# Optimization experiments

Measured on AMD Instinct MI355X. Metric: run time of the kernel, lower is better.

Reference implementation:

```python
import jax, jax.numpy as jnp
import numpy as np


def _prelu(x, a):
    # nn.PReLU() with a single learnable parameter a
    return jnp.where(x >= 0, x, a * x)


def _conv1x1(x, w, b):
    # x: [n, cin, h, w], w: [cout, cin], b: [cout]
    return jnp.einsum('nchw,oc->nohw', x, w) + b[None, :, None, None]


def setup_inputs() -> dict:
    key = jax.random.key(0)
    ks = jax.random.split(key, 7)
    N, C, H, W = 8, 64, 64, 64
    red = 2
    c = C // red
    s = 1.0 / np.sqrt(C).astype(np.float32)
    x = jax.random.normal(ks[0], (N, C, H, W), dtype=jnp.float32)
    w1 = jax.random.normal(ks[1], (c, C), dtype=jnp.float32) * s
    b1 = jnp.zeros((c,), dtype=jnp.float32)
    w2 = jax.random.normal(ks[2], (c, C), dtype=jnp.float32) * s
    b2 = jnp.zeros((c,), dtype=jnp.float32)
    w3 = jax.random.normal(ks[3], (C, C), dtype=jnp.float32) * s
    b3 = jnp.zeros((C,), dtype=jnp.float32)
    a1 = jnp.full((1,), 0.25, dtype=jnp.float32)
    a2 = jnp.full((1,), 0.25, dtype=jnp.float32)
    a3 = jnp.full((1,), 0.25, dtype=jnp.float32)
    return {"x": x, "w1": w1, "b1": b1, "a1": a1, "w2": w2, "b2": b2,
            "a2": a2, "w3": w3, "b3": b3, "a3": a3}


def reference(x, w1, b1, a1, w2, b2, a2, w3, b3, a3):
    res_scale = 1.0
    n, C, h, w = x.shape
    e1 = _prelu(_conv1x1(x, w1, b1), a1[0])  # [n, c, h, w]
    e2 = _prelu(_conv1x1(x, w2, b2), a2[0])  # [n, c, h, w]
    e3 = _prelu(_conv1x1(x, w3, b3), a3[0])  # [n, C, h, w]
    c = e1.shape[1]
    hw = h * w
    q = e1.transpose(0, 2, 3, 1).reshape(n, hw, c)   # [n, hw, c]
    k = e2.reshape(n, c, hw)                         # [n, c, hw]
    score = jax.nn.softmax(jnp.matmul(q, k), axis=-1)  # [n, hw, hw]
    v = e3.reshape(n, C, hw).transpose(0, 2, 1)      # [n, hw, C]
    out = jnp.matmul(score, v)                       # [n, hw, C]
    out = out.transpose(0, 2, 1).reshape(n, C, h, w)
    return out + res_scale * x
```

## Files before the change

### kernel.cpp

```cpp
#include <hip/hip_runtime.h>
#include <hip/hip_bf16.h>

typedef __bf16 bf16x8 __attribute__((ext_vector_type(8)));
typedef float  f32x4  __attribute__((ext_vector_type(4)));
typedef float  f32x16 __attribute__((ext_vector_type(16)));
typedef int    i32x4  __attribute__((ext_vector_type(4)));

#define SEQ 4096
#define CIN 64
#define KSPLIT 8
#define KCHUNK (SEQ / KSPLIT)
#define NT32 (KCHUNK / 32)
#define LOG2E 1.44269504088896340736f

__device__ __forceinline__ unsigned cvtpk(float lo, float hi) {
    unsigned r;
    asm("v_cvt_pk_bf16_f32 %0, %1, %2" : "=v"(r) : "v"(lo), "v"(hi));
    return r;
}

__global__ __launch_bounds__(256, 2) void qkv_gen(
    const float* __restrict__ x,
    const float* __restrict__ w1, const float* __restrict__ b1, const float* __restrict__ a1,
    const float* __restrict__ w2, const float* __restrict__ b2, const float* __restrict__ a2,
    const float* __restrict__ w3, const float* __restrict__ b3, const float* __restrict__ a3,
    __bf16* __restrict__ qws, __bf16* __restrict__ kws, __bf16* __restrict__ vtws)
{
    __shared__ float xs[CIN][64];
    __shared__ float wl[CIN][128];
    __shared__ float bl[128];
    __shared__ float al[4];

    const int t  = threadIdx.x;
    const int n  = blockIdx.x >> 6;
    const int p0 = (blockIdx.x & 63) << 6;

    for (int idx = t; idx < 2048; idx += 256) {
        int j = idx >> 6, c = idx & 63;
        wl[c][j]      = w1[idx];
        wl[c][32 + j] = w2[idx];
    }
    for (int idx = t; idx < 4096; idx += 256) {
        int j = idx >> 6, c = idx & 63;
        wl[c][64 + j] = w3[idx];
    }
    if (t < 32) { bl[t] = b1[t]; bl[32 + t] = b2[t]; }
    if (t >= 128 && t < 192) bl[64 + (t - 128)] = b3[t - 128];
    if (t == 0) { al[0] = a1[0]; al[1] = a2[0]; al[2] = a3[0]; }

    const float* xb = x + ((size_t)n * CIN) * SEQ + p0;
    for (int r = 0; r < 16; ++r) {
        int e = r * 256 + t;
        xs[e >> 6][e & 63] = xb[(size_t)(e >> 6) * SEQ + (e & 63)];
    }
    __syncthreads();

    const int p  = t & 63;
    const int g  = t >> 6;
    const int jb = g << 5;
    const float a = (g == 0) ? al[0] : ((g == 1) ? al[1] : al[2]);

    float acc[32];
    #pragma unroll
    for (int j = 0; j < 32; ++j) acc[j] = bl[jb + j];

    for (int c = 0; c < CIN; ++c) {
        float xv = xs[c][p];
        const f32x4* wr = (const f32x4*)&wl[c][jb];
        #pragma unroll
        for (int j4 = 0; j4 < 8; ++j4) {
            f32x4 wv = wr[j4];
            acc[j4*4+0] = fmaf(wv[0], xv, acc[j4*4+0]);
            acc[j4*4+1] = fmaf(wv[1], xv, acc[j4*4+1]);
            acc[j4*4+2] = fmaf(wv[2], xv, acc[j4*4+2]);
            acc[j4*4+3] = fmaf(wv[3], xv, acc[j4*4+3]);
        }
    }
    #pragma unroll
    for (int j = 0; j < 32; ++j) acc[j] = acc[j] >= 0.f ? acc[j] : a * acc[j];

    const int pg = p0 + p;
    if (g <= 1) {
        const float sc = (g == 0) ? LOG2E : 1.0f;
        __bf16* dst = (g == 0 ? qws : kws) + ((size_t)n * SEQ + pg) * 32;
        #pragma unroll
        for (int v8 = 0; v8 < 4; ++v8) {
            bf16x8 o;
            #pragma unroll
            for (int i = 0; i < 8; ++i) o[i] = (__bf16)(acc[v8*8+i] * sc);
            *(bf16x8*)(dst + v8*8) = o;
        }
    } else {
        __bf16* dst = vtws + (size_t)n * (256 * 1024)
                      + (size_t)(pg >> 4) * 1024 + (jb - 64) * 16 + (pg & 15);
        #pragma unroll
        for (int j = 0; j < 32; ++j) dst[j * 16] = (__bf16)acc[j];
    }
}

template<int ATOMIC>
__global__ __launch_bounds__(256, 4) void attn(
    const __bf16* __restrict__ qws, const __bf16* __restrict__ kws,
    const __bf16* __restrict__ vtws,
    void* __restrict__ Ows, float* __restrict__ lws)
{
    const int t    = threadIdx.x;
    const int lane = t & 63;
    const int n    = blockIdx.x & 7;
    const int qblk = (blockIdx.x >> 3) & 31;
    const int ks   = blockIdx.x >> 8;
    const int wid  = t >> 6;
    const int l31  = lane & 31;
    const int h    = lane >> 5;
    const int qbase = qblk * 128 + wid * 32;
    const int kbase = ks * KCHUNK;
    const int koff = l31 * 64 + h * 16;
    const int voff = l31 * 32 + h * 16;

    const char* kb = (const char*)(kws + (size_t)n * SEQ * 32) + (size_t)kbase * 64;
    const char* vb = (const char*)(vtws + (size_t)n * (256 * 1024))
                     + (size_t)(kbase >> 4) * 2048;

    const char* qp = (const char*)(qws + (size_t)n * SEQ * 32)
                     + (size_t)(qbase + l31) * 64 + h * 16;
    const bf16x8 qf0 = *(const bf16x8*)(qp);
    const bf16x8 qf1 = *(const bf16x8*)(qp + 32);

    f32x16 of0 = {}, of1 = {};
    f32x4 ls4 = {0.f, 0.f, 0.f, 0.f};

    #pragma unroll 2
    for (int tile = 0; tile < NT32; ++tile) {
        const char* kp = kb + (size_t)tile * 2048;
        const char* vp = vb + (size_t)tile * 4096;

        bf16x8 kfa  = *(const bf16x8*)(kp + koff);
        bf16x8 kfb  = *(const bf16x8*)(kp + koff + 32);
        bf16x8 vf00 = *(const bf16x8*)(vp + voff);
        bf16x8 vf01 = *(const bf16x8*)(vp + voff + 1024);
        bf16x8 vf10 = *(const bf16x8*)(vp + voff + 2048);
        bf16x8 vf11 = *(const bf16x8*)(vp + voff + 3072);

        f32x16 s = {};
        s = __builtin_amdgcn_mfma_f32_32x32x16_bf16(kfa, qf0, s, 0, 0, 0);
        s = __builtin_amdgcn_mfma_f32_32x32x16_bf16(kfb, qf1, s, 0, 0, 0);

        float p[16];
        #pragma unroll
        for (int r = 0; r < 16; ++r) p[r] = __builtin_exp2f(s[r]);
        f32x4 e0 = { p[0], p[1], p[2],  p[3]  };
        f32x4 e1 = { p[4], p[5], p[6],  p[7]  };
        f32x4 e2 = { p[8], p[9], p[10], p[11] };
        f32x4 e3 = { p[12], p[13], p[14], p[15] };
        ls4 += e0 + e1 + e2 + e3;

        unsigned c[8];
        #pragma unroll
        for (int j = 0; j < 4; ++j) {
            c[j]     = cvtpk(p[2*j],     p[2*j + 1]);
            c[4 + j] = cvtpk(p[8 + 2*j], p[9 + 2*j]);
        }
        asm("v_permlane32_swap_b32 %0, %1" : "+v"(c[0]), "+v"(c[2]));
        asm("v_permlane32_swap_b32 %0, %1" : "+v"(c[1]), "+v"(c[3]));
        asm("v_permlane32_swap_b32 %0, %1" : "+v"(c[4]), "+v"(c[6]));
        asm("v_permlane32_swap_b32 %0, %1" : "+v"(c[5]), "+v"(c[7]));

        i32x4 b0 = { (int)c[0], (int)c[1], (int)c[2], (int)c[3] };
        i32x4 b1 = { (int)c[4], (int)c[5], (int)c[6], (int)c[7] };
        bf16x8 pf0 = __builtin_bit_cast(bf16x8, b0);
        bf16x8 pf1 = __builtin_bit_cast(bf16x8, b1);
        of0 = __builtin_amdgcn_mfma_f32_32x32x16_bf16(vf00, pf0, of0, 0, 0, 0);
        of1 = __builtin_amdgcn_mfma_f32_32x32x16_bf16(vf01, pf0, of1, 0, 0, 0);
        of0 = __builtin_amdgcn_mfma_f32_32x32x16_bf16(vf10, pf1, of0, 0, 0, 0);
        of1 = __builtin_amdgcn_mfma_f32_32x32x16_bf16(vf11, pf1, of1, 0, 0, 0);
    }

    const float ls = ls4[0] + ls4[1] + ls4[2] + ls4[3];
    const int qg = qbase + l31;
    if (ATOMIC) {
        float* Ob = (float*)Ows + (size_t)n * CIN * SEQ;
        #pragma unroll
        for (int r = 0; r < 16; ++r) {
            int dv = (r & 3) + 8 * (r >> 2) + 4 * h;
            unsafeAtomicAdd(Ob + (size_t)dv * SEQ + qg,        of0[r]);
            unsafeAtomicAdd(Ob + (size_t)(dv + 32) * SEQ + qg, of1[r]);
        }
        unsafeAtomicAdd(lws + n * SEQ + qg, ls);
    } else {
        __bf16* Ob = (__bf16*)Ows + (size_t)ks * (8 * CIN * SEQ) + (size_t)n * CIN * SEQ;
        #pragma unroll
        for (int r = 0; r < 16; ++r) {
            int dv = (r & 3) + 8 * (r >> 2) + 4 * h;
            Ob[(size_t)dv * SEQ + qg]        = (__bf16)of0[r];
            Ob[(size_t)(dv + 32) * SEQ + qg] = (__bf16)of1[r];
        }
        float lt = ls + __shfl_xor(ls, 32);
        if (h == 0) lws[(size_t)ks * (8 * SEQ) + n * SEQ + qg] = lt;
    }
}

__global__ __launch_bounds__(256) void lred(float* __restrict__ lws)
{
    int i = blockIdx.x * 256 + threadIdx.x;
    float s = 0.f;
    #pragma unroll
    for (int ks = 0; ks < KSPLIT; ++ks) s += lws[ks * 32768 + i];
    lws[i] = 1.f / s;
}

__global__ __launch_bounds__(256) void combine8(
    const __bf16* __restrict__ O8, const float* __restrict__ linv,
    const float* __restrict__ x, float* __restrict__ out)
{
    const int i = blockIdx.x * 256 + threadIdx.x;
    const int q8 = i & 511;
    const int nd = i >> 9;
    const int n  = nd >> 6;

    float o[8] = {};
    const __bf16* base = O8 + (size_t)nd * SEQ + q8 * 8;
    #pragma unroll
    for (int ks = 0; ks < KSPLIT; ++ks) {
        bf16x8 v = *(const bf16x8*)(base + (size_t)ks * (8 * CIN * SEQ));
        #pragma unroll
        for (int j = 0; j < 8; ++j) o[j] += (float)v[j];
    }
    const float* ivp = linv + n * SEQ + q8 * 8;
    f32x4 iv0 = *(const f32x4*)(ivp);
    f32x4 iv1 = *(const f32x4*)(ivp + 4);
    const float* xp = x + (size_t)nd * SEQ + q8 * 8;
    f32x4 x0 = *(const f32x4*)(xp);
    f32x4 x1 = *(const f32x4*)(xp + 4);
    f32x4 r0, r1;
    r0[0] = o[0]*iv0[0] + x0[0]; r0[1] = o[1]*iv0[1] + x0[1];
    r0[2] = o[2]*iv0[2] + x0[2]; r0[3] = o[3]*iv0[3] + x0[3];
    r1[0] = o[4]*iv1[0] + x1[0]; r1[1] = o[5]*iv1[1] + x1[1];
    r1[2] = o[6]*iv1[2] + x1[2]; r1[3] = o[7]*iv1[3] + x1[3];
    float* op = out + (size_t)nd * SEQ + q8 * 8;
    *(f32x4*)(op)     = r0;
    *(f32x4*)(op + 4) = r1;
}

__global__ __launch_bounds__(256) void combine1(
    const float* __restrict__ Ows, const float* __restrict__ lws,
    const float* __restrict__ x, float* __restrict__ out)
{
    const int total = 8 * CIN * SEQ / 4;
    for (int i = blockIdx.x * 256 + threadIdx.x; i < total; i += gridDim.x * 256) {
        int q4 = i & 1023;
        int n  = i >> 16;
        f32x4 o4 = *(const f32x4*)(Ows + (size_t)i * 4);
        f32x4 l4 = *(const f32x4*)(lws + (size_t)n * SEQ + q4 * 4);
        f32x4 x4 = *(const f32x4*)(x + (size_t)i * 4);
        f32x4 r;
        r[0] = o4[0] / l4[0] + x4[0];
        r[1] = o4[1] / l4[1] + x4[1];
        r[2] = o4[2] / l4[2] + x4[2];
        r[3] = o4[3] / l4[3] + x4[3];
        *(f32x4*)(out + (size_t)i * 4) = r;
    }
}

extern "C" void kernel_launch(void* const* d_in, const int* in_sizes, int n_in,
                              void* d_out, int out_size, void* d_ws, size_t ws_size,
                              hipStream_t stream)
{
    (void)in_sizes; (void)n_in; (void)out_size;
    const float* x  = (const float*)d_in[0];
    const float* w1 = (const float*)d_in[1];
    const float* b1 = (const float*)d_in[2];
    const float* a1 = (const float*)d_in[3];
    const float* w2 = (const float*)d_in[4];
    const float* b2 = (const float*)d_in[5];
    const float* a2 = (const float*)d_in[6];
    const float* w3 = (const float*)d_in[7];
    const float* b3 = (const float*)d_in[8];
    const float* a3 = (const float*)d_in[9];
    float* out = (float*)d_out;

    char* ws = (char*)d_ws;
    __bf16* qws  = (__bf16*)(ws);
    __bf16* kws  = (__bf16*)(ws + (2u << 20));
    __bf16* vtws = (__bf16*)(ws + (4u << 20));

    hipLaunchKernelGGL(qkv_gen, dim3(512), dim3(256), 0, stream,
                       x, w1, b1, a1, w2, b2, a2, w3, b3, a3, qws, kws, vtws);

    const size_t need_split = (8u << 20) + (32u << 20) + (1u << 20);
    if (ws_size >= need_split) {
        __bf16* O8   = (__bf16*)(ws + (8u << 20));
        float*  lws8 = (float*)(ws + (40u << 20));
        hipLaunchKernelGGL(attn<0>, dim3(8 * 32 * KSPLIT), dim3(256), 0, stream,
                           qws, kws, vtws, (void*)O8, lws8);
        hipLaunchKernelGGL(lred, dim3(128), dim3(256), 0, stream, lws8);
        hipLaunchKernelGGL(combine8, dim3(1024), dim3(256), 0, stream,
                           O8, lws8, x, out);
    } else {
        float* Ows = (float*)(ws + (8u << 20));
        float* lws = (float*)(ws + (16u << 20));
        hipMemsetAsync(Ows, 0, (8u << 20) + (128u << 10), stream);
        hipLaunchKernelGGL(attn<1>, dim3(8 * 32 * KSPLIT), dim3(256), 0, stream,
                           qws, kws, vtws, (void*)Ows, lws);
        hipLaunchKernelGGL(combine1, dim3(1024), dim3(256), 0, stream,
                           Ows, lws, x, out);
    }
}
```

Before: 83.51 us.

## Software-pipeline attention K/V loads, raise MFMA priority, fold lred into combine

The attention inner loop now double-buffers its K/V fragment loads, issuing the next tile's global loads before computing the current tile, in place of a plain unroll-by-2. The MFMA sections are wrapped in s_setprio so matrix work gets scheduling priority over other waves. The separate row-sum reduction kernel is removed, and combine8 now sums the eight partial softmax denominators itself and divides directly. This saves one launch and one pass over lws, at the cost of more loads and divides per combine thread and higher register pressure from holding two fragment sets.

```diff
diff --git a/kernel.cpp b/kernel.cpp
--- a/kernel.cpp
+++ b/kernel.cpp
@@ -96,6 +96,25 @@
         #pragma unroll
         for (int j = 0; j < 32; ++j) dst[j * 16] = (__bf16)acc[j];
     }
+}
+
+struct Frags {
+    bf16x8 ka, kb, v00, v01, v10, v11;
+};
+
+__device__ __forceinline__ Frags ldf(const char* kb_, const char* vb_,
+                                     int tile, int koff, int voff)
+{
+    Frags f;
+    const char* kp = kb_ + (size_t)tile * 2048;
+    const char* vp = vb_ + (size_t)tile * 4096;
+    f.ka  = *(const bf16x8*)(kp + koff);
+    f.kb  = *(const bf16x8*)(kp + koff + 32);
+    f.v00 = *(const bf16x8*)(vp + voff);
+    f.v01 = *(const bf16x8*)(vp + voff + 1024);
+    f.v10 = *(const bf16x8*)(vp + voff + 2048);
+    f.v11 = *(const bf16x8*)(vp + voff + 3072);
+    return f;
 }
 
 template<int ATOMIC>
@@ -129,21 +148,12 @@
     f32x16 of0 = {}, of1 = {};
     f32x4 ls4 = {0.f, 0.f, 0.f, 0.f};
 
-    #pragma unroll 2
-    for (int tile = 0; tile < NT32; ++tile) {
-        const char* kp = kb + (size_t)tile * 2048;
-        const char* vp = vb + (size_t)tile * 4096;
-
-        bf16x8 kfa  = *(const bf16x8*)(kp + koff);
-        bf16x8 kfb  = *(const bf16x8*)(kp + koff + 32);
-        bf16x8 vf00 = *(const bf16x8*)(vp + voff);
-        bf16x8 vf01 = *(const bf16x8*)(vp + voff + 1024);
-        bf16x8 vf10 = *(const bf16x8*)(vp + voff + 2048);
-        bf16x8 vf11 = *(const bf16x8*)(vp + voff + 3072);
-
+    auto body = [&](const Frags& F) {
         f32x16 s = {};
-        s = __builtin_amdgcn_mfma_f32_32x32x16_bf16(kfa, qf0, s, 0, 0, 0);
-        s = __builtin_amdgcn_mfma_f32_32x32x16_bf16(kfb, qf1, s, 0, 0, 0);
+        __builtin_amdgcn_s_setprio(1);
+        s = __builtin_amdgcn_mfma_f32_32x32x16_bf16(F.ka, qf0, s, 0, 0, 0);
+        s = __builtin_amdgcn_mfma_f32_32x32x16_bf16(F.kb, qf1, s, 0, 0, 0);
+        __builtin_amdgcn_s_setprio(0);
 
         float p[16];
         #pragma unroll
@@ -169,10 +179,22 @@
         i32x4 b1 = { (int)c[4], (int)c[5], (int)c[6], (int)c[7] };
         bf16x8 pf0 = __builtin_bit_cast(bf16x8, b0);
         bf16x8 pf1 = __builtin_bit_cast(bf16x8, b1);
-        of0 = __builtin_amdgcn_mfma_f32_32x32x16_bf16(vf00, pf0, of0, 0, 0, 0);
-        of1 = __builtin_amdgcn_mfma_f32_32x32x16_bf16(vf01, pf0, of1, 0, 0, 0);
-        of0 = __builtin_amdgcn_mfma_f32_32x32x16_bf16(vf10, pf1, of0, 0, 0, 0);
-        of1 = __builtin_amdgcn_mfma_f32_32x32x16_bf16(vf11, pf1, of1, 0, 0, 0);
+        __builtin_amdgcn_s_setprio(1);
+        of0 = __builtin_amdgcn_mfma_f32_32x32x16_bf16(F.v00, pf0, of0, 0, 0, 0);
+        of1 = __builtin_amdgcn_mfma_f32_32x32x16_bf16(F.v01, pf0, of1, 0, 0, 0);
+        of0 = __builtin_amdgcn_mfma_f32_32x32x16_bf16(F.v10, pf1, of0, 0, 0, 0);
+        of1 = __builtin_amdgcn_mfma_f32_32x32x16_bf16(F.v11, pf1, of1, 0, 0, 0);
+        __builtin_amdgcn_s_setprio(0);
+    };
+
+    Frags A = ldf(kb, vb, 0, koff, voff);
+    #pragma unroll 1
+    for (int tile = 0; tile < NT32; tile += 2) {
+        Frags B = ldf(kb, vb, tile + 1, koff, voff);
+        body(A);
+        if (tile + 2 < NT32)
+            A = ldf(kb, vb, tile + 2, koff, voff);
+        body(B);
     }
 
     const float ls = ls4[0] + ls4[1] + ls4[2] + ls4[3];
@@ -199,17 +221,8 @@
     }
 }
 
-__global__ __launch_bounds__(256) void lred(float* __restrict__ lws)
-{
-    int i = blockIdx.x * 256 + threadIdx.x;
-    float s = 0.f;
-    #pragma unroll
-    for (int ks = 0; ks < KSPLIT; ++ks) s += lws[ks * 32768 + i];
-    lws[i] = 1.f / s;
-}
-
 __global__ __launch_bounds__(256) void combine8(
-    const __bf16* __restrict__ O8, const float* __restrict__ linv,
+    const __bf16* __restrict__ O8, const float* __restrict__ lws,
     const float* __restrict__ x, float* __restrict__ out)
 {
     const int i = blockIdx.x * 256 + threadIdx.x;
@@ -225,17 +238,25 @@
         #pragma unroll
         for (int j = 0; j < 8; ++j) o[j] += (float)v[j];
     }
-    const float* ivp = linv + n * SEQ + q8 * 8;
-    f32x4 iv0 = *(const f32x4*)(ivp);
-    f32x4 iv1 = *(const f32x4*)(ivp + 4);
+
+    float lsum[8] = {};
+    const float* lp = lws + n * SEQ + q8 * 8;
+    #pragma unroll
+    for (int ks = 0; ks < KSPLIT; ++ks) {
+        f32x4 a = *(const f32x4*)(lp + ks * 32768);
+        f32x4 b = *(const f32x4*)(lp + ks * 32768 + 4);
+        lsum[0] += a[0]; lsum[1] += a[1]; lsum[2] += a[2]; lsum[3] += a[3];
+        lsum[4] += b[0]; lsum[5] += b[1]; lsum[6] += b[2]; lsum[7] += b[3];
+    }
+
     const float* xp = x + (size_t)nd * SEQ + q8 * 8;
     f32x4 x0 = *(const f32x4*)(xp);
     f32x4 x1 = *(const f32x4*)(xp + 4);
     f32x4 r0, r1;
-    r0[0] = o[0]*iv0[0] + x0[0]; r0[1] = o[1]*iv0[1] + x0[1];
-    r0[2] = o[2]*iv0[2] + x0[2]; r0[3] = o[3]*iv0[3] + x0[3];
-    r1[0] = o[4]*iv1[0] + x1[0]; r1[1] = o[5]*iv1[1] + x1[1];
-    r1[2] = o[6]*iv1[2] + x1[2]; r1[3] = o[7]*iv1[3] + x1[3];
+    r0[0] = o[0]/lsum[0] + x0[0]; r0[1] = o[1]/lsum[1] + x0[1];
+    r0[2] = o[2]/lsum[2] + x0[2]; r0[3] = o[3]/lsum[3] + x0[3];
+    r1[0] = o[4]/lsum[4] + x1[0]; r1[1] = o[5]/lsum[5] + x1[1];
+    r1[2] = o[6]/lsum[6] + x1[2]; r1[3] = o[7]/lsum[7] + x1[3];
     float* op = out + (size_t)nd * SEQ + q8 * 8;
     *(f32x4*)(op)     = r0;
     *(f32x4*)(op + 4) = r1;
@@ -292,7 +313,6 @@
         float*  lws8 = (float*)(ws + (40u << 20));
         hipLaunchKernelGGL(attn<0>, dim3(8 * 32 * KSPLIT), dim3(256), 0, stream,
                            qws, kws, vtws, (void*)O8, lws8);
-        hipLaunchKernelGGL(lred, dim3(128), dim3(256), 0, stream, lws8);
         hipLaunchKernelGGL(combine8, dim3(1024), dim3(256), 0, stream,
                            O8, lws8, x, out);
     } else {
```

After: 82.37 us. About the same (-1.4%).
